# Kernel tuning notes

Hardware: AMD Instinct MI355X
Metric: run time of the kernel (lower is better)

Reference implementation:

```python
import jax, jax.numpy as jnp
import numpy as np

DIM = 256
NUM_HEADS = 8
HEAD_DIM = DIM // NUM_HEADS


def setup_inputs() -> dict:
    key = jax.random.key(0)
    k1, k2, k3, k4 = jax.random.split(key, 4)
    B, C, H, W = 16, DIM, 64, 64
    x = jax.random.normal(k1, (B, C, H, W), dtype=jnp.float32)
    # 1x1 convs as dense weight matrices [out_ch, in_ch]
    Wqkv = jax.random.normal(k2, (3 * DIM, DIM), dtype=jnp.float32) * (DIM ** -0.5)
    Wproj = jax.random.normal(k3, (DIM, DIM), dtype=jnp.float32) * (DIM ** -0.5)
    bproj = jax.random.normal(k4, (DIM,), dtype=jnp.float32) * 0.01
    return {"x": x, "Wqkv": Wqkv, "Wproj": Wproj, "bproj": bproj}


def reference(x, Wqkv, Wproj, bproj):
    B, C, H, W = x.shape
    N = H * W
    hd = C // NUM_HEADS

    # qkv: 1x1 conv (no bias) == channel matmul
    qkv = jnp.einsum('oc,bchw->bohw', Wqkv, x)  # [B, 3C, H, W]
    q, k, v = jnp.split(qkv, 3, axis=1)

    def to_heads(t):
        # b (h d) x y -> b h (x y) d
        return t.reshape(B, NUM_HEADS, hd, N).transpose(0, 1, 3, 2)

    q, k, v = to_heads(q), to_heads(k), to_heads(v)  # [B, h, N, d]

    # linear attention feature map + per-token normalization over d
    q = jax.nn.elu(q) + 1.0
    k = jax.nn.elu(k) + 1.0
    q = q / jnp.sum(q, axis=-1, keepdims=True)
    k = k / jnp.sum(k, axis=-1, keepdims=True)

    kv = jnp.einsum('bhnd,bhne->bhde', k, v)   # [B, h, d, d]
    out = jnp.einsum('bhnd,bhde->bhne', q, kv)  # [B, h, N, d]

    # b h (x y) d -> b (h d) x y
    out = out.transpose(0, 1, 3, 2).reshape(B, C, H, W)

    # proj: 1x1 conv with bias; drop_path is identity in eval mode
    out = jnp.einsum('oc,bchw->bohw', Wproj, out) + bproj[None, :, None, None]
    return out + x
```

## Files before the change

### kernel.cpp

```cpp
#include <hip/hip_runtime.h>
#include <stdint.h>
#include <stddef.h>

#define DIM   256
#define NH    8
#define HD    32
#define BATCH 16
#define NTOK  4096

typedef __attribute__((ext_vector_type(8))) short short8;
typedef __attribute__((ext_vector_type(4))) float f32x4;

__device__ __forceinline__ unsigned short f2bf(float x){
  unsigned u = __float_as_uint(x);
  u += 0x7fffu + ((u >> 16) & 1u);
  return (unsigned short)(u >> 16);
}
__device__ __forceinline__ float bf2f(unsigned short h){
  return __uint_as_float(((unsigned)h) << 16);
}
__device__ __forceinline__ float elu1(float v){
  return (v > 0.f) ? (v + 1.f) : __expf(v);
}
__device__ __forceinline__ void gload_lds16(const void* g, void* lds){
  __builtin_amdgcn_global_load_lds(
      (const __attribute__((address_space(1))) unsigned int*)g,
      (__attribute__((address_space(3))) unsigned int*)lds, 16, 0, 0);
}

__global__ __launch_bounds__(256) void k_transpose_x(const float* __restrict__ x,
                                                     unsigned short* __restrict__ xt){
  __shared__ float tile[64][65];
  const int b = blockIdx.z, c0 = blockIdx.y * 64, n0 = blockIdx.x * 64;
  const float* xb = x + (size_t)b * DIM * NTOK;
  const int t = threadIdx.x;
  #pragma unroll
  for (int p = 0; p < 4; p++){
    int idx = t + p * 256;
    int row = idx >> 4;
    int col = (idx & 15) << 2;
    float4 v = *(const float4*)(xb + (size_t)(c0 + row) * NTOK + n0 + col);
    tile[row][col] = v.x; tile[row][col+1] = v.y; tile[row][col+2] = v.z; tile[row][col+3] = v.w;
  }
  __syncthreads();
  unsigned short* xtb = xt + (size_t)b * NTOK * DIM;
  #pragma unroll
  for (int p = 0; p < 4; p++){
    int idx = t + p * 256;
    int nl = idx >> 4;
    int cl = (idx & 15) << 2;
    ushort4 o;
    o.x = f2bf(tile[cl+0][nl]); o.y = f2bf(tile[cl+1][nl]);
    o.z = f2bf(tile[cl+2][nl]); o.w = f2bf(tile[cl+3][nl]);
    *(ushort4*)(xtb + (size_t)(n0 + nl) * DIM + c0 + cl) = o;
  }
}

__global__ __launch_bounds__(256) void k_convert_w(const float* __restrict__ wqkv,
                                                   unsigned short* __restrict__ wq_bf){
  int i = blockIdx.x * 256 + threadIdx.x;
  float4 v = *(const float4*)(wqkv + (size_t)i * 4);
  ushort4 o = { f2bf(v.x), f2bf(v.y), f2bf(v.z), f2bf(v.w) };
  *(ushort4*)(wq_bf + (size_t)i * 4) = o;
}

__global__ __launch_bounds__(256) void k_qkv2(const unsigned short* __restrict__ wbf,
                                              const unsigned short* __restrict__ xt,
                                              unsigned short* __restrict__ qn,
                                              unsigned short* __restrict__ kvT){
  __shared__ __align__(16) unsigned short sh[17408];
  unsigned short* As = sh;
  unsigned short* Bs = sh + 8192;
  const int t = threadIdx.x;
  const int w = t >> 6, l = t & 63;
  const int t16 = l & 15, quad = l >> 4;
  const int wm = w >> 1, wn = w & 1;
  const int bid = blockIdx.x;
  const int otile = bid >> 9;
  const int nb = bid & 511;
  const int nt = nb >> 4, b = nb & 15;
  const int o0 = otile * 128, n0 = nt * 128;
  const unsigned short* A = wbf;
  const unsigned short* B = xt + (size_t)b * NTOK * DIM;

  f32x4 acc[4][4];
  #pragma unroll
  for (int i = 0; i < 4; i++)
    #pragma unroll
    for (int j = 0; j < 4; j++){ acc[i][j][0]=0.f; acc[i][j][1]=0.f; acc[i][j][2]=0.f; acc[i][j][3]=0.f; }

  for (int k0 = 0; k0 < 256; k0 += 64){
    __syncthreads();
    #pragma unroll
    for (int j = 0; j < 4; j++){
      int s = w * 4 + j;
      int tile = s >> 1, kk = s & 1;
      gload_lds16(A + (size_t)(o0 + tile*16 + t16) * DIM + k0 + kk*32 + quad*8, As + s * 512);
      gload_lds16(B + (size_t)(n0 + tile*16 + t16) * DIM + k0 + kk*32 + quad*8, Bs + s * 512);
    }
    __syncthreads();
    #pragma unroll
    for (int kk = 0; kk < 2; kk++){
      short8 a[4], bb[4];
      #pragma unroll
      for (int i = 0; i < 4; i++) a[i]  = *(const short8*)(As + ((wm*4 + i)*2 + kk) * 512 + l * 8);
      #pragma unroll
      for (int j = 0; j < 4; j++) bb[j] = *(const short8*)(Bs + ((wn*4 + j)*2 + kk) * 512 + l * 8);
      #pragma unroll
      for (int i = 0; i < 4; i++)
        #pragma unroll
        for (int j = 0; j < 4; j++)
          acc[i][j] = __builtin_amdgcn_mfma_f32_16x16x32_bf16(a[i], bb[j], acc[i][j], 0, 0, 0);
    }
  }
  __syncthreads();

  const bool isV = (o0 >= 512);
  const bool isQ = (o0 < 256);
  if (!isV){
    #pragma unroll
    for (int i = 0; i < 4; i++)
      #pragma unroll
      for (int j = 0; j < 4; j++)
        #pragma unroll
        for (int r = 0; r < 4; r++) acc[i][j][r] = elu1(acc[i][j][r]);
    float s[2][4];
    #pragma unroll
    for (int hi = 0; hi < 2; hi++)
      #pragma unroll
      for (int j = 0; j < 4; j++){
        float v = 0.f;
        #pragma unroll
        for (int ii = 0; ii < 2; ii++)
          #pragma unroll
          for (int r = 0; r < 4; r++) v += acc[hi*2 + ii][j][r];
        v += __shfl_xor(v, 16);
        v += __shfl_xor(v, 32);
        s[hi][j] = 1.0f / v;
      }
    #pragma unroll
    for (int i = 0; i < 4; i++)
      #pragma unroll
      for (int j = 0; j < 4; j++){
        float inv = s[i>>1][j];
        #pragma unroll
        for (int r = 0; r < 4; r++) acc[i][j][r] *= inv;
      }
  }

  if (isQ){
    #pragma unroll
    for (int i = 0; i < 4; i++)
      #pragma unroll
      for (int j = 0; j < 4; j++){
        int n_l = wn*64 + j*16 + t16;
        #pragma unroll
        for (int r = 0; r < 4; r++){
          int o_l = wm*64 + i*16 + quad*4 + r;
          sh[n_l*136 + o_l] = f2bf(acc[i][j][r]);
        }
      }
  } else {
    #pragma unroll
    for (int i = 0; i < 4; i++)
      #pragma unroll
      for (int j = 0; j < 4; j++){
        int n_l = wn*64 + j*16 + t16;
        #pragma unroll
        for (int r = 0; r < 4; r++){
          int o_l = wm*64 + i*16 + quad*4 + r;
          sh[o_l*136 + n_l] = f2bf(acc[i][j][r]);
        }
      }
  }
  __syncthreads();

  if (isQ){
    unsigned short* dst = qn + (size_t)b * NTOK * DIM;
    #pragma unroll
    for (int p = 0; p < 8; p++){
      int g = t + p * 256;
      int n_l = g >> 4, c = g & 15;
      uint4 v = *(const uint4*)(sh + n_l*136 + c*8);
      *(uint4*)(dst + (size_t)(n0 + n_l) * DIM + o0 + c*8) = v;
    }
  } else {
    unsigned short* dst = kvT + (size_t)b * 512 * NTOK + (size_t)(o0 - 256) * NTOK;
    #pragma unroll
    for (int p = 0; p < 8; p++){
      int g = t + p * 256;
      int o_l = g >> 4, c = g & 15;
      uint4 v = *(const uint4*)(sh + o_l*136 + c*8);
      *(uint4*)(dst + (size_t)o_l * NTOK + n0 + c*8) = v;
    }
  }
}

__global__ __launch_bounds__(256) void k_kv2(const unsigned short* __restrict__ kvT,
                                             float* __restrict__ kvp){
  const int t = threadIdx.x;
  const int w = t >> 6, l = t & 63;
  const int t16 = l & 15, quad = l >> 4;
  const int ns = blockIdx.x, h = blockIdx.y, b = blockIdx.z;
  const unsigned short* base = kvT + (size_t)b * 512 * NTOK;
  const int n_off = ns * 1024 + w * 256;

  f32x4 acc[2][2];
  #pragma unroll
  for (int i = 0; i < 2; i++)
    #pragma unroll
    for (int j = 0; j < 2; j++){ acc[i][j][0]=0.f; acc[i][j][1]=0.f; acc[i][j][2]=0.f; acc[i][j][3]=0.f; }

  const unsigned short* krow0 = base + (size_t)(h*32 + t16) * NTOK;
  const unsigned short* krow1 = krow0 + (size_t)16 * NTOK;
  const unsigned short* vrow0 = base + (size_t)(256 + h*32 + t16) * NTOK;
  const unsigned short* vrow1 = vrow0 + (size_t)16 * NTOK;

  for (int kk = 0; kk < 8; kk++){
    int n = n_off + kk*32 + quad*8;
    short8 a0 = *(const short8*)(krow0 + n);
    short8 a1 = *(const short8*)(krow1 + n);
    short8 b0 = *(const short8*)(vrow0 + n);
    short8 b1 = *(const short8*)(vrow1 + n);
    acc[0][0] = __builtin_amdgcn_mfma_f32_16x16x32_bf16(a0, b0, acc[0][0], 0, 0, 0);
    acc[0][1] = __builtin_amdgcn_mfma_f32_16x16x32_bf16(a0, b1, acc[0][1], 0, 0, 0);
    acc[1][0] = __builtin_amdgcn_mfma_f32_16x16x32_bf16(a1, b0, acc[1][0], 0, 0, 0);
    acc[1][1] = __builtin_amdgcn_mfma_f32_16x16x32_bf16(a1, b1, acc[1][1], 0, 0, 0);
  }
  float* dst = kvp + (size_t)(((b*8 + h)*16) + ns*4 + w) * 1024;
  #pragma unroll
  for (int ti = 0; ti < 2; ti++)
    #pragma unroll
    for (int tj = 0; tj < 2; tj++)
      #pragma unroll
      for (int r = 0; r < 4; r++)
        dst[(ti*16 + quad*4 + r)*32 + tj*16 + t16] = acc[ti][tj][r];
}

__global__ __launch_bounds__(256) void k_M(const float* __restrict__ kvp,
                                           const float* __restrict__ wproj,
                                           unsigned short* __restrict__ M){
  __shared__ float kvL[1024];
  __shared__ float wpL[8192];
  const int t = threadIdx.x;
  const int h = blockIdx.x, b = blockIdx.y;
  const float* pbase = kvp + (size_t)((b*8 + h)*16) * 1024;
  {
    float4 a = {0.f,0.f,0.f,0.f};
    #pragma unroll
    for (int p = 0; p < 16; p++){
      float4 v = *(const float4*)(pbase + (size_t)p*1024 + t*4);
      a.x += v.x; a.y += v.y; a.z += v.z; a.w += v.w;
    }
    *(float4*)(kvL + t*4) = a;
  }
  #pragma unroll
  for (int p = 0; p < 8; p++){
    int idx = t + p * 256;
    int o = idx >> 3, e4 = idx & 7;
    *(float4*)(wpL + o*32 + e4*4) = *(const float4*)(wproj + (size_t)o * DIM + h*32 + e4*4);
  }
  __syncthreads();
  float wr[32];
  #pragma unroll
  for (int e = 0; e < 32; e++) wr[e] = wpL[t*32 + e];
  unsigned short md[32];
  #pragma unroll
  for (int d = 0; d < 32; d++){
    float a = 0.f;
    #pragma unroll
    for (int e = 0; e < 32; e++) a += wr[e] * kvL[d*32 + e];
    md[d] = f2bf(a);
  }
  unsigned short* dst = M + (size_t)b * 65536 + (size_t)t * DIM + h*32;
  #pragma unroll
  for (int q = 0; q < 4; q++) *(uint4*)(dst + q*8) = *(const uint4*)(md + q*8);
}

__global__ __launch_bounds__(256) void k_out(const unsigned short* __restrict__ M,
                                             const unsigned short* __restrict__ qn,
                                             const float* __restrict__ x,
                                             const float* __restrict__ bproj,
                                             float* __restrict__ out){
  __shared__ __align__(16) unsigned short As[8192];
  __shared__ __align__(16) unsigned short Bs[8192];
  const int t = threadIdx.x;
  const int w = t >> 6, l = t & 63;
  const int t16 = l & 15, quad = l >> 4;
  const int wm = w >> 1, wn = w & 1;
  const int b = blockIdx.z;
  const int n0 = blockIdx.y * 128, o0 = blockIdx.x * 128;
  const unsigned short* A = M + (size_t)b * 65536;
  const unsigned short* B = qn + (size_t)b * NTOK * DIM;

  f32x4 acc[4][4];
  #pragma unroll
  for (int i = 0; i < 4; i++)
    #pragma unroll
    for (int j = 0; j < 4; j++){ acc[i][j][0]=0.f; acc[i][j][1]=0.f; acc[i][j][2]=0.f; acc[i][j][3]=0.f; }

  for (int k0 = 0; k0 < 256; k0 += 64){
    __syncthreads();
    #pragma unroll
    for (int j = 0; j < 4; j++){
      int s = w * 4 + j;
      int tile = s >> 1, kk = s & 1;
      gload_lds16(A + (size_t)(o0 + tile*16 + t16) * DIM + k0 + kk*32 + quad*8, As + s * 512);
      gload_lds16(B + (size_t)(n0 + tile*16 + t16) * DIM + k0 + kk*32 + quad*8, Bs + s * 512);
    }
    __syncthreads();
    #pragma unroll
    for (int kk = 0; kk < 2; kk++){
      short8 a[4], bb[4];
      #pragma unroll
      for (int i = 0; i < 4; i++) a[i]  = *(const short8*)(As + ((wm*4 + i)*2 + kk) * 512 + l * 8);
      #pragma unroll
      for (int j = 0; j < 4; j++) bb[j] = *(const short8*)(Bs + ((wn*4 + j)*2 + kk) * 512 + l * 8);
      #pragma unroll
      for (int i = 0; i < 4; i++)
        #pragma unroll
        for (int j = 0; j < 4; j++)
          acc[i][j] = __builtin_amdgcn_mfma_f32_16x16x32_bf16(a[i], bb[j], acc[i][j], 0, 0, 0);
    }
  }

  const float* xb = x + (size_t)b * DIM * NTOK;
  float* ob = out + (size_t)b * DIM * NTOK;
  #pragma unroll
  for (int i = 0; i < 4; i++){
    #pragma unroll
    for (int r = 0; r < 4; r++){
      int o = o0 + wm*64 + i*16 + quad*4 + r;
      float bias = bproj[o];
      #pragma unroll
      for (int j = 0; j < 4; j++){
        int n = n0 + wn*64 + j*16 + t16;
        float v = acc[i][j][r] + bias + xb[(size_t)o * NTOK + n];
        ob[(size_t)o * NTOK + n] = v;
      }
    }
  }
}

extern "C" void kernel_launch(void* const* d_in, const int* in_sizes, int n_in,
                              void* d_out, int out_size, void* d_ws, size_t ws_size,
                              hipStream_t stream){
  const float* x     = (const float*)d_in[0];
  const float* wqkv  = (const float*)d_in[1];
  const float* wproj = (const float*)d_in[2];
  const float* bproj = (const float*)d_in[3];
  float* out = (float*)d_out;
  char* ws = (char*)d_ws;

  unsigned short* xt   = (unsigned short*)(ws);
  unsigned short* qn   = (unsigned short*)(ws + ((size_t)32 << 20));
  unsigned short* kvT  = (unsigned short*)(ws + ((size_t)64 << 20));
  unsigned short* wqbf = (unsigned short*)(ws + ((size_t)128 << 20));
  float* kvp = (float*)(ws);
  unsigned short* M = (unsigned short*)(ws + ((size_t)8 << 20));

  k_transpose_x<<<dim3(64, 4, 16), 256, 0, stream>>>(x, xt);
  k_convert_w  <<<dim3(192), 256, 0, stream>>>(wqkv, wqbf);
  k_qkv2       <<<dim3(3072), 256, 0, stream>>>(wqbf, xt, qn, kvT);
  k_kv2        <<<dim3(4, 8, 16), 256, 0, stream>>>(kvT, kvp);
  k_M          <<<dim3(8, 16), 256, 0, stream>>>(kvp, wproj, M);
  k_out        <<<dim3(2, 32, 16), 256, 0, stream>>>(M, qn, x, bproj, out);
}
```

Measured before the change: 260.9 us.

## Load GEMM operands straight from global memory, regroup block order, split kv reduction

In the qkv and output-projection GEMMs, the LDS staging through global_load_lds and its __syncthreads barriers is removed. Each wave now reads its own MFMA fragments directly from global memory and relies on L2 for reuse. Block indices are remapped into super-groups so blocks sharing the same input tile run close together, and both GEMMs get launch_bounds with 3 blocks per CU. The kv partial reduction is split twice as finely for more parallelism, and the partial buffer and M offset are adjusted to match. The risk is heavier global and L2 traffic and less coalesced fragment loads in exchange for removing the barriers.

```diff
diff --git a/kernel.cpp b/kernel.cpp
--- a/kernel.cpp
+++ b/kernel.cpp
@@ -21,11 +21,6 @@
 }
 __device__ __forceinline__ float elu1(float v){
   return (v > 0.f) ? (v + 1.f) : __expf(v);
-}
-__device__ __forceinline__ void gload_lds16(const void* g, void* lds){
-  __builtin_amdgcn_global_load_lds(
-      (const __attribute__((address_space(1))) unsigned int*)g,
-      (__attribute__((address_space(3))) unsigned int*)lds, 16, 0, 0);
 }
 
 __global__ __launch_bounds__(256) void k_transpose_x(const float* __restrict__ x,
@@ -64,24 +59,25 @@
   *(ushort4*)(wq_bf + (size_t)i * 4) = o;
 }
 
-__global__ __launch_bounds__(256) void k_qkv2(const unsigned short* __restrict__ wbf,
-                                              const unsigned short* __restrict__ xt,
-                                              unsigned short* __restrict__ qn,
-                                              unsigned short* __restrict__ kvT){
+__global__ __launch_bounds__(256, 3) void k_qkv3(const unsigned short* __restrict__ wbf,
+                                                 const unsigned short* __restrict__ xt,
+                                                 unsigned short* __restrict__ qn,
+                                                 unsigned short* __restrict__ kvT){
   __shared__ __align__(16) unsigned short sh[17408];
-  unsigned short* As = sh;
-  unsigned short* Bs = sh + 8192;
   const int t = threadIdx.x;
   const int w = t >> 6, l = t & 63;
   const int t16 = l & 15, quad = l >> 4;
   const int wm = w >> 1, wn = w & 1;
   const int bid = blockIdx.x;
-  const int otile = bid >> 9;
-  const int nb = bid & 511;
-  const int nt = nb >> 4, b = nb & 15;
-  const int o0 = otile * 128, n0 = nt * 128;
-  const unsigned short* A = wbf;
-  const unsigned short* B = xt + (size_t)b * NTOK * DIM;
+  const int super = bid / 48;
+  const int rem = bid - super * 48;
+  const int m = rem >> 3, lx = rem & 7;
+  const int g = super * 8 + lx;
+  const int nt = g >> 4, b = g & 15;
+  const int o0 = m * 128, n0 = nt * 128;
+
+  const unsigned short* A  = wbf + (size_t)(o0 + wm*64) * DIM;
+  const unsigned short* Bp = xt + (size_t)b * NTOK * DIM + (size_t)(n0 + wn*64) * DIM;
 
   f32x4 acc[4][4];
   #pragma unroll
@@ -89,31 +85,20 @@
     #pragma unroll
     for (int j = 0; j < 4; j++){ acc[i][j][0]=0.f; acc[i][j][1]=0.f; acc[i][j][2]=0.f; acc[i][j][3]=0.f; }
 
-  for (int k0 = 0; k0 < 256; k0 += 64){
-    __syncthreads();
-    #pragma unroll
-    for (int j = 0; j < 4; j++){
-      int s = w * 4 + j;
-      int tile = s >> 1, kk = s & 1;
-      gload_lds16(A + (size_t)(o0 + tile*16 + t16) * DIM + k0 + kk*32 + quad*8, As + s * 512);
-      gload_lds16(B + (size_t)(n0 + tile*16 + t16) * DIM + k0 + kk*32 + quad*8, Bs + s * 512);
-    }
-    __syncthreads();
-    #pragma unroll
-    for (int kk = 0; kk < 2; kk++){
-      short8 a[4], bb[4];
-      #pragma unroll
-      for (int i = 0; i < 4; i++) a[i]  = *(const short8*)(As + ((wm*4 + i)*2 + kk) * 512 + l * 8);
-      #pragma unroll
-      for (int j = 0; j < 4; j++) bb[j] = *(const short8*)(Bs + ((wn*4 + j)*2 + kk) * 512 + l * 8);
-      #pragma unroll
-      for (int i = 0; i < 4; i++)
-        #pragma unroll
-        for (int j = 0; j < 4; j++)
-          acc[i][j] = __builtin_amdgcn_mfma_f32_16x16x32_bf16(a[i], bb[j], acc[i][j], 0, 0, 0);
-    }
-  }
-  __syncthreads();
+  #pragma unroll
+  for (int kc = 0; kc < 8; kc++){
+    const int ko = kc * 32 + quad * 8;
+    short8 a[4], bb[4];
+    #pragma unroll
+    for (int i = 0; i < 4; i++) a[i]  = *(const short8*)(A  + (size_t)(i*16 + t16) * DIM + ko);
+    #pragma unroll
+    for (int j = 0; j < 4; j++) bb[j] = *(const short8*)(Bp + (size_t)(j*16 + t16) * DIM + ko);
+    #pragma unroll
+    for (int i = 0; i < 4; i++)
+      #pragma unroll
+      for (int j = 0; j < 4; j++)
+        acc[i][j] = __builtin_amdgcn_mfma_f32_16x16x32_bf16(a[i], bb[j], acc[i][j], 0, 0, 0);
+  }
 
   const bool isV = (o0 >= 512);
   const bool isQ = (o0 < 256);
@@ -179,8 +164,8 @@
     unsigned short* dst = qn + (size_t)b * NTOK * DIM;
     #pragma unroll
     for (int p = 0; p < 8; p++){
-      int g = t + p * 256;
-      int n_l = g >> 4, c = g & 15;
+      int gg = t + p * 256;
+      int n_l = gg >> 4, c = gg & 15;
       uint4 v = *(const uint4*)(sh + n_l*136 + c*8);
       *(uint4*)(dst + (size_t)(n0 + n_l) * DIM + o0 + c*8) = v;
     }
@@ -188,8 +173,8 @@
     unsigned short* dst = kvT + (size_t)b * 512 * NTOK + (size_t)(o0 - 256) * NTOK;
     #pragma unroll
     for (int p = 0; p < 8; p++){
-      int g = t + p * 256;
-      int o_l = g >> 4, c = g & 15;
+      int gg = t + p * 256;
+      int o_l = gg >> 4, c = gg & 15;
       uint4 v = *(const uint4*)(sh + o_l*136 + c*8);
       *(uint4*)(dst + (size_t)o_l * NTOK + n0 + c*8) = v;
     }
@@ -203,7 +188,7 @@
   const int t16 = l & 15, quad = l >> 4;
   const int ns = blockIdx.x, h = blockIdx.y, b = blockIdx.z;
   const unsigned short* base = kvT + (size_t)b * 512 * NTOK;
-  const int n_off = ns * 1024 + w * 256;
+  const int n_off = ns * 512 + w * 128;
 
   f32x4 acc[2][2];
   #pragma unroll
@@ -216,7 +201,8 @@
   const unsigned short* vrow0 = base + (size_t)(256 + h*32 + t16) * NTOK;
   const unsigned short* vrow1 = vrow0 + (size_t)16 * NTOK;
 
-  for (int kk = 0; kk < 8; kk++){
+  #pragma unroll
+  for (int kk = 0; kk < 4; kk++){
     int n = n_off + kk*32 + quad*8;
     short8 a0 = *(const short8*)(krow0 + n);
     short8 a1 = *(const short8*)(krow1 + n);
@@ -227,7 +213,7 @@
     acc[1][0] = __builtin_amdgcn_mfma_f32_16x16x32_bf16(a1, b0, acc[1][0], 0, 0, 0);
     acc[1][1] = __builtin_amdgcn_mfma_f32_16x16x32_bf16(a1, b1, acc[1][1], 0, 0, 0);
   }
-  float* dst = kvp + (size_t)(((b*8 + h)*16) + ns*4 + w) * 1024;
+  float* dst = kvp + (size_t)(((b*8 + h)*32) + ns*4 + w) * 1024;
   #pragma unroll
   for (int ti = 0; ti < 2; ti++)
     #pragma unroll
@@ -244,11 +230,11 @@
   __shared__ float wpL[8192];
   const int t = threadIdx.x;
   const int h = blockIdx.x, b = blockIdx.y;
-  const float* pbase = kvp + (size_t)((b*8 + h)*16) * 1024;
+  const float* pbase = kvp + (size_t)((b*8 + h)*32) * 1024;
   {
     float4 a = {0.f,0.f,0.f,0.f};
     #pragma unroll
-    for (int p = 0; p < 16; p++){
+    for (int p = 0; p < 32; p++){
       float4 v = *(const float4*)(pbase + (size_t)p*1024 + t*4);
       a.x += v.x; a.y += v.y; a.z += v.z; a.w += v.w;
     }
@@ -277,21 +263,25 @@
   for (int q = 0; q < 4; q++) *(uint4*)(dst + q*8) = *(const uint4*)(md + q*8);
 }
 
-__global__ __launch_bounds__(256) void k_out(const unsigned short* __restrict__ M,
-                                             const unsigned short* __restrict__ qn,
-                                             const float* __restrict__ x,
-                                             const float* __restrict__ bproj,
-                                             float* __restrict__ out){
-  __shared__ __align__(16) unsigned short As[8192];
-  __shared__ __align__(16) unsigned short Bs[8192];
+__global__ __launch_bounds__(256, 3) void k_out3(const unsigned short* __restrict__ M,
+                                                 const unsigned short* __restrict__ qn,
+                                                 const float* __restrict__ x,
+                                                 const float* __restrict__ bproj,
+                                                 float* __restrict__ out){
   const int t = threadIdx.x;
   const int w = t >> 6, l = t & 63;
   const int t16 = l & 15, quad = l >> 4;
   const int wm = w >> 1, wn = w & 1;
-  const int b = blockIdx.z;
-  const int n0 = blockIdx.y * 128, o0 = blockIdx.x * 128;
-  const unsigned short* A = M + (size_t)b * 65536;
-  const unsigned short* B = qn + (size_t)b * NTOK * DIM;
+  const int bid = blockIdx.x;
+  const int super = bid >> 4;
+  const int rem = bid & 15;
+  const int m = rem >> 3, lx = rem & 7;
+  const int g = super * 8 + lx;
+  const int nt = g >> 4, b = g & 15;
+  const int o0 = m * 128, n0 = nt * 128;
+
+  const unsigned short* A  = M + (size_t)b * 65536 + (size_t)(o0 + wm*64) * DIM;
+  const unsigned short* Bp = qn + (size_t)b * NTOK * DIM + (size_t)(n0 + wn*64) * DIM;
 
   f32x4 acc[4][4];
   #pragma unroll
@@ -299,29 +289,19 @@
     #pragma unroll
     for (int j = 0; j < 4; j++){ acc[i][j][0]=0.f; acc[i][j][1]=0.f; acc[i][j][2]=0.f; acc[i][j][3]=0.f; }
 
-  for (int k0 = 0; k0 < 256; k0 += 64){
-    __syncthreads();
-    #pragma unroll
-    for (int j = 0; j < 4; j++){
-      int s = w * 4 + j;
-      int tile = s >> 1, kk = s & 1;
-      gload_lds16(A + (size_t)(o0 + tile*16 + t16) * DIM + k0 + kk*32 + quad*8, As + s * 512);
-      gload_lds16(B + (size_t)(n0 + tile*16 + t16) * DIM + k0 + kk*32 + quad*8, Bs + s * 512);
-    }
-    __syncthreads();
-    #pragma unroll
-    for (int kk = 0; kk < 2; kk++){
-      short8 a[4], bb[4];
-      #pragma unroll
-      for (int i = 0; i < 4; i++) a[i]  = *(const short8*)(As + ((wm*4 + i)*2 + kk) * 512 + l * 8);
-      #pragma unroll
-      for (int j = 0; j < 4; j++) bb[j] = *(const short8*)(Bs + ((wn*4 + j)*2 + kk) * 512 + l * 8);
-      #pragma unroll
-      for (int i = 0; i < 4; i++)
-        #pragma unroll
-        for (int j = 0; j < 4; j++)
-          acc[i][j] = __builtin_amdgcn_mfma_f32_16x16x32_bf16(a[i], bb[j], acc[i][j], 0, 0, 0);
-    }
+  #pragma unroll
+  for (int kc = 0; kc < 8; kc++){
+    const int ko = kc * 32 + quad * 8;
+    short8 a[4], bb[4];
+    #pragma unroll
+    for (int i = 0; i < 4; i++) a[i]  = *(const short8*)(A  + (size_t)(i*16 + t16) * DIM + ko);
+    #pragma unroll
+    for (int j = 0; j < 4; j++) bb[j] = *(const short8*)(Bp + (size_t)(j*16 + t16) * DIM + ko);
+    #pragma unroll
+    for (int i = 0; i < 4; i++)
+      #pragma unroll
+      for (int j = 0; j < 4; j++)
+        acc[i][j] = __builtin_amdgcn_mfma_f32_16x16x32_bf16(a[i], bb[j], acc[i][j], 0, 0, 0);
   }
 
   const float* xb = x + (size_t)b * DIM * NTOK;
@@ -357,12 +337,12 @@
   unsigned short* kvT  = (unsigned short*)(ws + ((size_t)64 << 20));
   unsigned short* wqbf = (unsigned short*)(ws + ((size_t)128 << 20));
   float* kvp = (float*)(ws);
-  unsigned short* M = (unsigned short*)(ws + ((size_t)8 << 20));
+  unsigned short* M = (unsigned short*)(ws + ((size_t)16 << 20));
 
   k_transpose_x<<<dim3(64, 4, 16), 256, 0, stream>>>(x, xt);
   k_convert_w  <<<dim3(192), 256, 0, stream>>>(wqkv, wqbf);
-  k_qkv2       <<<dim3(3072), 256, 0, stream>>>(wqbf, xt, qn, kvT);
-  k_kv2        <<<dim3(4, 8, 16), 256, 0, stream>>>(kvT, kvp);
+  k_qkv3       <<<dim3(3072), 256, 0, stream>>>(wqbf, xt, qn, kvT);
+  k_kv2        <<<dim3(8, 8, 16), 256, 0, stream>>>(kvT, kvp);
   k_M          <<<dim3(8, 16), 256, 0, stream>>>(kvp, wproj, M);
-  k_out        <<<dim3(2, 32, 16), 256, 0, stream>>>(M, qn, x, bproj, out);
-}
+  k_out3       <<<dim3(1024), 256, 0, stream>>>(M, qn, x, bproj, out);
+}
```

Result: slower. 304.4 us (+16.7%).

## Fuse KV outer-product into QKV GEMM epilogue and swizzle block order

Applied to the files above, without the earlier changes.

Weight rows are reordered so that each 128-row output tile holds the K and V channels of the same two heads. The QKV GEMM can then compute per-tile partial K^T V products straight from shared memory and write fp32 partials. This removes the kvT bf16 round trip through global memory and the separate k_kv2 kernel. It costs more partials for k_M to reduce, 32 per head instead of 16. Block indices in both GEMMs are also remapped into supergroups so that blocks sharing the same xt/qn tiles run close together, which should improve L2 reuse.

```diff
diff --git a/kernel.cpp b/kernel.cpp
--- a/kernel.cpp
+++ b/kernel.cpp
@@ -15,9 +15,6 @@
   unsigned u = __float_as_uint(x);
   u += 0x7fffu + ((u >> 16) & 1u);
   return (unsigned short)(u >> 16);
-}
-__device__ __forceinline__ float bf2f(unsigned short h){
-  return __uint_as_float(((unsigned)h) << 16);
 }
 __device__ __forceinline__ float elu1(float v){
   return (v > 0.f) ? (v + 1.f) : __expf(v);
@@ -59,15 +56,21 @@
 __global__ __launch_bounds__(256) void k_convert_w(const float* __restrict__ wqkv,
                                                    unsigned short* __restrict__ wq_bf){
   int i = blockIdx.x * 256 + threadIdx.x;
-  float4 v = *(const float4*)(wqkv + (size_t)i * 4);
+  int row = i >> 6;
+  int c4 = (i & 63) * 4;
+  int dst;
+  if (row < 256)      dst = row;
+  else if (row < 512){ int p = (row - 256) >> 6; int s = (row - 256) & 63; dst = 256 + p*128 + s; }
+  else               { int p = (row - 512) >> 6; int s = (row - 512) & 63; dst = 256 + p*128 + 64 + s; }
+  float4 v = *(const float4*)(wqkv + (size_t)row * DIM + c4);
   ushort4 o = { f2bf(v.x), f2bf(v.y), f2bf(v.z), f2bf(v.w) };
-  *(ushort4*)(wq_bf + (size_t)i * 4) = o;
-}
-
-__global__ __launch_bounds__(256) void k_qkv2(const unsigned short* __restrict__ wbf,
+  *(ushort4*)(wq_bf + (size_t)dst * DIM + c4) = o;
+}
+
+__global__ __launch_bounds__(256) void k_qkv4(const unsigned short* __restrict__ wbf,
                                               const unsigned short* __restrict__ xt,
                                               unsigned short* __restrict__ qn,
-                                              unsigned short* __restrict__ kvT){
+                                              float* __restrict__ kvp){
   __shared__ __align__(16) unsigned short sh[17408];
   unsigned short* As = sh;
   unsigned short* Bs = sh + 8192;
@@ -76,10 +79,12 @@
   const int t16 = l & 15, quad = l >> 4;
   const int wm = w >> 1, wn = w & 1;
   const int bid = blockIdx.x;
-  const int otile = bid >> 9;
-  const int nb = bid & 511;
-  const int nt = nb >> 4, b = nb & 15;
-  const int o0 = otile * 128, n0 = nt * 128;
+  const int super = bid / 48;
+  const int rem = bid - super * 48;
+  const int m = rem >> 3, lx = rem & 7;
+  const int g = super * 8 + lx;
+  const int nt = g >> 4, b = g & 15;
+  const int o0 = m * 128, n0 = nt * 128;
   const unsigned short* A = wbf;
   const unsigned short* B = xt + (size_t)b * NTOK * DIM;
 
@@ -115,9 +120,8 @@
   }
   __syncthreads();
 
-  const bool isV = (o0 >= 512);
   const bool isQ = (o0 < 256);
-  if (!isV){
+  if (isQ || wm == 0){
     #pragma unroll
     for (int i = 0; i < 4; i++)
       #pragma unroll
@@ -179,62 +183,36 @@
     unsigned short* dst = qn + (size_t)b * NTOK * DIM;
     #pragma unroll
     for (int p = 0; p < 8; p++){
-      int g = t + p * 256;
-      int n_l = g >> 4, c = g & 15;
+      int gg = t + p * 256;
+      int n_l = gg >> 4, c = gg & 15;
       uint4 v = *(const uint4*)(sh + n_l*136 + c*8);
       *(uint4*)(dst + (size_t)(n0 + n_l) * DIM + o0 + c*8) = v;
     }
   } else {
-    unsigned short* dst = kvT + (size_t)b * 512 * NTOK + (size_t)(o0 - 256) * NTOK;
-    #pragma unroll
-    for (int p = 0; p < 8; p++){
-      int g = t + p * 256;
-      int o_l = g >> 4, c = g & 15;
-      uint4 v = *(const uint4*)(sh + o_l*136 + c*8);
-      *(uint4*)(dst + (size_t)o_l * NTOK + n0 + c*8) = v;
-    }
-  }
-}
-
-__global__ __launch_bounds__(256) void k_kv2(const unsigned short* __restrict__ kvT,
-                                             float* __restrict__ kvp){
-  const int t = threadIdx.x;
-  const int w = t >> 6, l = t & 63;
-  const int t16 = l & 15, quad = l >> 4;
-  const int ns = blockIdx.x, h = blockIdx.y, b = blockIdx.z;
-  const unsigned short* base = kvT + (size_t)b * 512 * NTOK;
-  const int n_off = ns * 1024 + w * 256;
-
-  f32x4 acc[2][2];
-  #pragma unroll
-  for (int i = 0; i < 2; i++)
-    #pragma unroll
-    for (int j = 0; j < 2; j++){ acc[i][j][0]=0.f; acc[i][j][1]=0.f; acc[i][j][2]=0.f; acc[i][j][3]=0.f; }
-
-  const unsigned short* krow0 = base + (size_t)(h*32 + t16) * NTOK;
-  const unsigned short* krow1 = krow0 + (size_t)16 * NTOK;
-  const unsigned short* vrow0 = base + (size_t)(256 + h*32 + t16) * NTOK;
-  const unsigned short* vrow1 = vrow0 + (size_t)16 * NTOK;
-
-  for (int kk = 0; kk < 8; kk++){
-    int n = n_off + kk*32 + quad*8;
-    short8 a0 = *(const short8*)(krow0 + n);
-    short8 a1 = *(const short8*)(krow1 + n);
-    short8 b0 = *(const short8*)(vrow0 + n);
-    short8 b1 = *(const short8*)(vrow1 + n);
-    acc[0][0] = __builtin_amdgcn_mfma_f32_16x16x32_bf16(a0, b0, acc[0][0], 0, 0, 0);
-    acc[0][1] = __builtin_amdgcn_mfma_f32_16x16x32_bf16(a0, b1, acc[0][1], 0, 0, 0);
-    acc[1][0] = __builtin_amdgcn_mfma_f32_16x16x32_bf16(a1, b0, acc[1][0], 0, 0, 0);
-    acc[1][1] = __builtin_amdgcn_mfma_f32_16x16x32_bf16(a1, b1, acc[1][1], 0, 0, 0);
-  }
-  float* dst = kvp + (size_t)(((b*8 + h)*16) + ns*4 + w) * 1024;
-  #pragma unroll
-  for (int ti = 0; ti < 2; ti++)
-    #pragma unroll
-    for (int tj = 0; tj < 2; tj++)
+    const int p = (o0 >> 7) - 2;
+    const int hl = w >> 1, eh = w & 1;
+    f32x4 kvacc[2];
+    kvacc[0][0]=0.f; kvacc[0][1]=0.f; kvacc[0][2]=0.f; kvacc[0][3]=0.f;
+    kvacc[1][0]=0.f; kvacc[1][1]=0.f; kvacc[1][2]=0.f; kvacc[1][3]=0.f;
+    const unsigned short* kbase = sh + (hl*32) * 136;
+    const unsigned short* vbase = sh + (64 + hl*32 + eh*16) * 136;
+    #pragma unroll
+    for (int kk = 0; kk < 4; kk++){
+      int nn = kk*32 + quad*8;
+      short8 bfrag = *(const short8*)(vbase + t16*136 + nn);
+      #pragma unroll
+      for (int ti = 0; ti < 2; ti++){
+        short8 afrag = *(const short8*)(kbase + (ti*16 + t16)*136 + nn);
+        kvacc[ti] = __builtin_amdgcn_mfma_f32_16x16x32_bf16(afrag, bfrag, kvacc[ti], 0, 0, 0);
+      }
+    }
+    float* dst = kvp + ((size_t)(b*8 + p*2 + hl) * 32 + nt) * 1024;
+    #pragma unroll
+    for (int ti = 0; ti < 2; ti++)
       #pragma unroll
       for (int r = 0; r < 4; r++)
-        dst[(ti*16 + quad*4 + r)*32 + tj*16 + t16] = acc[ti][tj][r];
+        dst[(ti*16 + quad*4 + r)*32 + eh*16 + t16] = kvacc[ti][r];
+  }
 }
 
 __global__ __launch_bounds__(256) void k_M(const float* __restrict__ kvp,
@@ -244,11 +222,11 @@
   __shared__ float wpL[8192];
   const int t = threadIdx.x;
   const int h = blockIdx.x, b = blockIdx.y;
-  const float* pbase = kvp + (size_t)((b*8 + h)*16) * 1024;
+  const float* pbase = kvp + (size_t)((b*8 + h)*32) * 1024;
   {
     float4 a = {0.f,0.f,0.f,0.f};
     #pragma unroll
-    for (int p = 0; p < 16; p++){
+    for (int p = 0; p < 32; p++){
       float4 v = *(const float4*)(pbase + (size_t)p*1024 + t*4);
       a.x += v.x; a.y += v.y; a.z += v.z; a.w += v.w;
     }
@@ -277,19 +255,24 @@
   for (int q = 0; q < 4; q++) *(uint4*)(dst + q*8) = *(const uint4*)(md + q*8);
 }
 
-__global__ __launch_bounds__(256) void k_out(const unsigned short* __restrict__ M,
-                                             const unsigned short* __restrict__ qn,
-                                             const float* __restrict__ x,
-                                             const float* __restrict__ bproj,
-                                             float* __restrict__ out){
+__global__ __launch_bounds__(256) void k_out4(const unsigned short* __restrict__ M,
+                                              const unsigned short* __restrict__ qn,
+                                              const float* __restrict__ x,
+                                              const float* __restrict__ bproj,
+                                              float* __restrict__ out){
   __shared__ __align__(16) unsigned short As[8192];
   __shared__ __align__(16) unsigned short Bs[8192];
   const int t = threadIdx.x;
   const int w = t >> 6, l = t & 63;
   const int t16 = l & 15, quad = l >> 4;
   const int wm = w >> 1, wn = w & 1;
-  const int b = blockIdx.z;
-  const int n0 = blockIdx.y * 128, o0 = blockIdx.x * 128;
+  const int bid = blockIdx.x;
+  const int super = bid >> 4;
+  const int rem = bid & 15;
+  const int m = rem >> 3, lx = rem & 7;
+  const int g = super * 8 + lx;
+  const int nt = g >> 4, b = g & 15;
+  const int o0 = m * 128, n0 = nt * 128;
   const unsigned short* A = M + (size_t)b * 65536;
   const unsigned short* B = qn + (size_t)b * NTOK * DIM;
 
@@ -354,15 +337,13 @@
 
   unsigned short* xt   = (unsigned short*)(ws);
   unsigned short* qn   = (unsigned short*)(ws + ((size_t)32 << 20));
-  unsigned short* kvT  = (unsigned short*)(ws + ((size_t)64 << 20));
-  unsigned short* wqbf = (unsigned short*)(ws + ((size_t)128 << 20));
-  float* kvp = (float*)(ws);
-  unsigned short* M = (unsigned short*)(ws + ((size_t)8 << 20));
+  float* kvp           = (float*)(ws + ((size_t)64 << 20));
+  unsigned short* M    = (unsigned short*)(ws + ((size_t)80 << 20));
+  unsigned short* wqbf = (unsigned short*)(ws + ((size_t)82 << 20));
 
   k_transpose_x<<<dim3(64, 4, 16), 256, 0, stream>>>(x, xt);
   k_convert_w  <<<dim3(192), 256, 0, stream>>>(wqkv, wqbf);
-  k_qkv2       <<<dim3(3072), 256, 0, stream>>>(wqbf, xt, qn, kvT);
-  k_kv2        <<<dim3(4, 8, 16), 256, 0, stream>>>(kvT, kvp);
+  k_qkv4       <<<dim3(3072), 256, 0, stream>>>(wqbf, xt, qn, kvp);
   k_M          <<<dim3(8, 16), 256, 0, stream>>>(kvp, wproj, M);
-  k_out        <<<dim3(2, 32, 16), 256, 0, stream>>>(M, qn, x, bproj, out);
-}
+  k_out4       <<<dim3(1024), 256, 0, stream>>>(M, qn, x, bproj, out);
+}
```

Measured after the change: 251.5 us. 1.04x faster.
